# Kernel tuning notes

Measured on AMD Instinct MI355X. Metric: run time of the kernel, lower is better.

The kernel has to match this reference:

```python
import jax, jax.numpy as jnp
import numpy as np

N = 8192


def setup_inputs() -> dict:
    key = jax.random.key(0)
    ks = jax.random.split(key, 12)
    H_emb = jax.random.normal(ks[0], (645, 1140), jnp.float32) * 0.05
    H_emb = H_emb.at[0].set(0.0)  # padding_idx=0
    inp = {
        "ld_gcn": jax.random.normal(ks[1], (N, 512), jnp.float32),
        "ld_encoder": jax.random.normal(ks[2], (N, 512), jnp.float32),
        "x": jax.random.randint(ks[3], (N,), 0, 240),
        "y": jax.random.randint(ks[4], (N,), 0, 404),
        "H_emb": H_emb,
        "conv_w": jax.random.normal(ks[5], (32, 1, 2, 25), jnp.float32) * (1.0 / np.sqrt(2 * 25)),
        "conv_b": jnp.zeros((32,), jnp.float32),
        "W1": jax.random.normal(ks[6], (1000, 3968), jnp.float32) * (1.0 / np.sqrt(3968)),
        "b1": jnp.zeros((1000,), jnp.float32),
        "W2": jax.random.normal(ks[7], (100, 1000), jnp.float32) * (1.0 / np.sqrt(1000)),
        "b2": jnp.zeros((100,), jnp.float32),
        "Wg": jax.random.normal(ks[8], (100, 512), jnp.float32) * (1.0 / np.sqrt(512)),
        "bg": jnp.zeros((100,), jnp.float32),
        "We": jax.random.normal(ks[9], (100, 512), jnp.float32) * (1.0 / np.sqrt(512)),
        "be": jnp.zeros((100,), jnp.float32),
    }
    return inp


def reference(ld_gcn, ld_encoder, x, y, H_emb, conv_w, conv_b, W1, b1, W2, b2, Wg, bg, We, be):
    n = x.shape[0]
    lrelu = lambda t: jax.nn.leaky_relu(t, 0.01)
    # embedding lookups + concat -> (n,1,2,1140)
    h = jnp.concatenate([H_emb[x], H_emb[y + 240]], axis=1).reshape(n, 1, 2, 1140)
    # CNN: conv (2,25) stride (1,9) valid -> (n,32,1,124)
    c = jax.lax.conv_general_dilated(h, conv_w, window_strides=(1, 9), padding="VALID",
                                     dimension_numbers=("NCHW", "OIHW", "NCHW"))
    c = lrelu(c + conv_b[None, :, None, None]).reshape(n, -1)  # (n,3968)
    # fc_H (dropout = identity at eval)
    hfc = lrelu(c @ W1.T + b1)
    hfc = lrelu(hfc @ W2.T + b2)  # (n,100)
    # gating projections
    g = jnp.tanh(ld_gcn @ Wg.T + bg)       # (n,100)
    e = jnp.tanh(ld_encoder @ We.T + be)   # (n,100)
    # diagonal of (n,100)@(100,n) == row-wise dot product
    a_gcn = jnp.einsum("nd,nd->n", g, hfc)
    a_enc = jnp.einsum("nd,nd->n", e, hfc)
    att = jax.nn.softmax(jnp.stack([a_gcn, a_enc], axis=1), axis=1)  # (n,2)
    return ld_gcn * att[:, :1], ld_encoder * att[:, 1:]
```

## Files before the change

### kernel.cpp

```cpp
#include <hip/hip_runtime.h>
#include <hip/hip_bf16.h>

typedef unsigned short u16;
typedef short bf16x8 __attribute__((ext_vector_type(8)));
typedef float f32x4 __attribute__((ext_vector_type(4)));

#define NROWS 8192
#define EMBD  1140
#define FDIM  3968
#define N1R   1000
#define N1P   1024
#define N2R   100
#define N2P   128
#define DG    512

__device__ inline u16 f2b(float f) {
  __hip_bfloat16 h = __float2bfloat16(f);
  return *reinterpret_cast<u16*>(&h);
}

__device__ inline float b2f(u16 u) {
  unsigned v = (unsigned)u << 16;
  union { unsigned u; float f; } c;
  c.u = v;
  return c.f;
}

__device__ inline float tanh_fast(float x) {
  float ax = fabsf(x);
  float t = __expf(-2.f * ax);
  float r = (1.f - t) / (1.f + t);
  return x < 0.f ? -r : r;
}

__device__ inline void gld16(const void* g, void* l) {
  __builtin_amdgcn_global_load_lds(
      (const __attribute__((address_space(1))) unsigned int*)g,
      (__attribute__((address_space(3))) unsigned int*)l, 16, 0, 0);
}

__global__ __launch_bounds__(256) void prep_kernel(
    const float* __restrict__ W1, const float* __restrict__ W2,
    const float* __restrict__ Wg, const float* __restrict__ We,
    const float* __restrict__ H_emb, const float* __restrict__ conv_w,
    const float* __restrict__ conv_b,
    u16* __restrict__ W1bf, u16* __restrict__ W2bf,
    u16* __restrict__ Wgbf, u16* __restrict__ Webf,
    u16* __restrict__ Abuf, u16* __restrict__ Bbuf) {
  const int b = blockIdx.x;
  const int t = threadIdx.x;
  if (b < 2112) {
    const float* src;
    u16* dst;
    int row, c8, realRow, realCol;
    if (b < 1984) {
      int id = b * 256 + t;
      row = id / 496; c8 = (id - row * 496) * 8;
      src = W1 + (size_t)row * FDIM + c8;
      dst = W1bf + (size_t)row * FDIM + c8;
      realRow = N1R; realCol = FDIM;
    } else if (b < 2048) {
      int id = (b - 1984) * 256 + t;
      row = id >> 7; c8 = (id & 127) * 8;
      src = W2 + (size_t)row * N1R + c8;
      dst = W2bf + (size_t)row * N1P + c8;
      realRow = N2R; realCol = N1R;
    } else if (b < 2080) {
      int id = (b - 2048) * 256 + t;
      row = id >> 6; c8 = (id & 63) * 8;
      src = Wg + (size_t)row * DG + c8;
      dst = Wgbf + (size_t)row * DG + c8;
      realRow = N2R; realCol = DG;
    } else {
      int id = (b - 2080) * 256 + t;
      row = id >> 6; c8 = (id & 63) * 8;
      src = We + (size_t)row * DG + c8;
      dst = Webf + (size_t)row * DG + c8;
      realRow = N2R; realCol = DG;
    }
    bf16x8 o = (bf16x8){0, 0, 0, 0, 0, 0, 0, 0};
    if (row < realRow && c8 < realCol) {
#pragma unroll
      for (int j = 0; j < 8; ++j) o[j] = (short)f2b(src[j]);
    }
    *(bf16x8*)dst = o;
    return;
  }
  __shared__ float se[EMBD];
  __shared__ float sw[32 * 25];
  __shared__ float sb[32];
  const int eb = b - 2112;
  bool isA = eb < 240;
  const float* emb = H_emb + (size_t)eb * EMBD;
  u16* outp = isA ? (Abuf + (size_t)eb * FDIM) : (Bbuf + (size_t)(eb - 240) * FDIM);
  for (int i = t; i < EMBD; i += 256) se[i] = emb[i];
  int kh = isA ? 0 : 1;
  for (int i = t; i < 800; i += 256) {
    int o = i / 25, kw = i - o * 25;
    sw[i] = conv_w[o * 50 + kh * 25 + kw];
  }
  if (t < 32) sb[t] = isA ? conv_b[t] : 0.f;
  __syncthreads();
  for (int f = t; f < FDIM; f += 256) {
    int o = f / 124, wpos = f - o * 124;
    const float* e = se + wpos * 9;
    const float* wp = sw + o * 25;
    float acc = sb[o];
#pragma unroll
    for (int kw = 0; kw < 25; ++kw) acc += wp[kw] * e[kw];
    outp[f] = f2b(acc);
  }
}

__global__ __launch_bounds__(256) void conv_combine_kernel(
    const u16* __restrict__ Abuf, const u16* __restrict__ Bbuf,
    const int* __restrict__ xi, const int* __restrict__ yi, u16* __restrict__ cbf) {
  int r = blockIdx.x;
  const bf16x8* pa = (const bf16x8*)(Abuf + (size_t)xi[r] * FDIM);
  const bf16x8* pb = (const bf16x8*)(Bbuf + (size_t)yi[r] * FDIM);
  bf16x8* out = (bf16x8*)(cbf + (size_t)r * FDIM);
  for (int i = threadIdx.x; i < FDIM / 8; i += 256) {
    bf16x8 a = pa[i], b = pb[i];
    bf16x8 o;
#pragma unroll
    for (int j = 0; j < 8; ++j) {
      float v = b2f((u16)a[j]) + b2f((u16)b[j]);
      v = v > 0.f ? v : 0.01f * v;
      o[j] = (short)f2b(v);
    }
    out[i] = o;
  }
}

__global__ __launch_bounds__(256) void fc1_kernel(
    const u16* __restrict__ A, const u16* __restrict__ B,
    const float* __restrict__ bias, int realN,
    u16* __restrict__ C, int K, int ldc, int nTilesX) {
  const int nwg = gridDim.x;
  const int cpx = nwg >> 3;
  const int bid = blockIdx.x;
  const int wg = (bid & 7) * cpx + (bid >> 3);
  const int tm = (wg / nTilesX) * 128;
  const int tn = (wg % nTilesX) * 128;

  __shared__ u16 As[2][8192];
  __shared__ u16 Bs[2][8192];
  const int t = threadIdx.x;
  const int lane = t & 63;
  const int w = t >> 6;
  const int wr = (w >> 1) * 64, wc = (w & 1) * 64;
  const int fr = lane & 15;
  const int kg = lane >> 4;

  const int srow = lane >> 3;
  const int su = ((lane & 7) ^ srow) * 8;
  const u16* gA[4];
  const u16* gB[4];
  int ldsOff[4];
#pragma unroll
  for (int i = 0; i < 4; ++i) {
    const int c = w + i * 4;
    gA[i] = A + (size_t)(tm + c * 8 + srow) * K + su;
    gB[i] = B + (size_t)(tn + c * 8 + srow) * K + su;
    ldsOff[i] = c * 512;
  }

  f32x4 acc[4][4];
#pragma unroll
  for (int m = 0; m < 4; ++m)
#pragma unroll
    for (int n = 0; n < 4; ++n) acc[m][n] = (f32x4){0.f, 0.f, 0.f, 0.f};

  const int nk = K >> 6;
#pragma unroll
  for (int i = 0; i < 4; ++i) {
    gld16(gA[i], &As[0][ldsOff[i]]);
    gld16(gB[i], &Bs[0][ldsOff[i]]);
  }
  __syncthreads();

  for (int kt = 0; kt < nk; ++kt) {
    const int cb = kt & 1;
    if (kt + 1 < nk) {
      const int ko = (kt + 1) << 6;
#pragma unroll
      for (int i = 0; i < 4; ++i) {
        gld16(gA[i] + ko, &As[cb ^ 1][ldsOff[i]]);
        gld16(gB[i] + ko, &Bs[cb ^ 1][ldsOff[i]]);
      }
    }
    __builtin_amdgcn_sched_barrier(0);
#pragma unroll
    for (int ks = 0; ks < 2; ++ks) {
      const int un = ((ks * 4 + kg) ^ (fr & 7)) << 4;
      bf16x8 af[4], bff[4];
#pragma unroll
      for (int m = 0; m < 4; ++m)
        af[m] = *(const bf16x8*)((const char*)As[cb] + (wr + m * 16 + fr) * 128 + un);
#pragma unroll
      for (int n = 0; n < 4; ++n)
        bff[n] = *(const bf16x8*)((const char*)Bs[cb] + (wc + n * 16 + fr) * 128 + un);
#pragma unroll
      for (int m = 0; m < 4; ++m)
#pragma unroll
        for (int n = 0; n < 4; ++n)
          acc[m][n] = __builtin_amdgcn_mfma_f32_16x16x32_bf16(af[m], bff[n], acc[m][n], 0, 0, 0);
    }
    __syncthreads();
  }

#pragma unroll
  for (int n = 0; n < 4; ++n) {
    int col = tn + wc + n * 16 + fr;
    float bv = (col < realN) ? bias[col] : 0.f;
#pragma unroll
    for (int m = 0; m < 4; ++m) {
#pragma unroll
      for (int j = 0; j < 4; ++j) {
        int row = tm + wr + m * 16 + kg * 4 + j;
        float v = acc[m][n][j] + bv;
        v = v > 0.f ? v : 0.01f * v;
        C[(size_t)row * ldc + col] = f2b(v);
      }
    }
  }
}

__global__ __launch_bounds__(256) void tail_kernel(
    const u16* __restrict__ hfc1, const u16* __restrict__ W2bf, const float* __restrict__ b2,
    const float* __restrict__ ldg, const float* __restrict__ lde,
    const u16* __restrict__ Wgbf, const float* __restrict__ bg,
    const u16* __restrict__ Webf, const float* __restrict__ be,
    float* __restrict__ out0, float* __restrict__ out1) {
  __shared__ float H16[N2P][16];
  __shared__ float dpart[2][4][16];
  __shared__ float wt[2][16];

  const int tm = blockIdx.x * 16;
  const int t = threadIdx.x;
  const int lane = t & 63;
  const int w = t >> 6;
  const int fr = lane & 15;
  const int kg = lane >> 4;
  const int n0 = w * 2;

  {
    f32x4 a0 = (f32x4){0.f, 0.f, 0.f, 0.f}, a1 = a0;
    const u16* Ap = hfc1 + (size_t)(tm + fr) * N1P + kg * 8;
    const u16* B0 = W2bf + (size_t)(n0 * 16 + fr) * N1P + kg * 8;
    const u16* B1 = B0 + (size_t)16 * N1P;
#pragma unroll 8
    for (int kt = 0; kt < N1P / 32; ++kt) {
      bf16x8 af = *(const bf16x8*)(Ap + kt * 32);
      bf16x8 f0 = *(const bf16x8*)(B0 + kt * 32);
      bf16x8 f1 = *(const bf16x8*)(B1 + kt * 32);
      a0 = __builtin_amdgcn_mfma_f32_16x16x32_bf16(af, f0, a0, 0, 0, 0);
      a1 = __builtin_amdgcn_mfma_f32_16x16x32_bf16(af, f1, a1, 0, 0, 0);
    }
#pragma unroll
    for (int n = 0; n < 2; ++n) {
      int col = (n0 + n) * 16 + fr;
      float bv = (col < N2R) ? b2[col] : 0.f;
      f32x4 v = n == 0 ? a0 : a1;
      f32x4 o;
#pragma unroll
      for (int j = 0; j < 4; ++j) {
        float x = v[j] + bv;
        o[j] = x > 0.f ? x : 0.01f * x;
      }
      *(f32x4*)&H16[col][kg * 4] = o;
    }
  }
  __syncthreads();

#pragma unroll 1
  for (int sec = 0; sec < 2; ++sec) {
    const float* ld = sec == 0 ? ldg : lde;
    const u16* Wb = sec == 0 ? Wgbf : Webf;
    const float* bb = sec == 0 ? bg : be;

    f32x4 a0 = (f32x4){0.f, 0.f, 0.f, 0.f}, a1 = a0;
    const float* Ap = ld + (size_t)(tm + fr) * DG + kg * 8;
    const u16* B0 = Wb + (size_t)(n0 * 16 + fr) * DG + kg * 8;
    const u16* B1 = B0 + (size_t)16 * DG;
#pragma unroll 4
    for (int kt = 0; kt < DG / 32; ++kt) {
      float4 v0 = *(const float4*)(Ap + kt * 32);
      float4 v1 = *(const float4*)(Ap + kt * 32 + 4);
      bf16x8 af;
      af[0] = (short)f2b(v0.x); af[1] = (short)f2b(v0.y);
      af[2] = (short)f2b(v0.z); af[3] = (short)f2b(v0.w);
      af[4] = (short)f2b(v1.x); af[5] = (short)f2b(v1.y);
      af[6] = (short)f2b(v1.z); af[7] = (short)f2b(v1.w);
      bf16x8 f0 = *(const bf16x8*)(B0 + kt * 32);
      bf16x8 f1 = *(const bf16x8*)(B1 + kt * 32);
      a0 = __builtin_amdgcn_mfma_f32_16x16x32_bf16(af, f0, a0, 0, 0, 0);
      a1 = __builtin_amdgcn_mfma_f32_16x16x32_bf16(af, f1, a1, 0, 0, 0);
    }
    float dv[4] = {0.f, 0.f, 0.f, 0.f};
#pragma unroll
    for (int n = 0; n < 2; ++n) {
      int col = (n0 + n) * 16 + fr;
      float bv = (col < N2R) ? bb[col] : 0.f;
      f32x4 v = n == 0 ? a0 : a1;
      f32x4 h = *(const f32x4*)&H16[col][kg * 4];
#pragma unroll
      for (int j = 0; j < 4; ++j)
        dv[j] += tanh_fast(v[j] + bv) * h[j];
    }
#pragma unroll
    for (int j = 0; j < 4; ++j) {
      float v = dv[j];
      v += __shfl_xor(v, 1);
      v += __shfl_xor(v, 2);
      v += __shfl_xor(v, 4);
      v += __shfl_xor(v, 8);
      dv[j] = v;
    }
    if (fr == 0) {
#pragma unroll
      for (int j = 0; j < 4; ++j) dpart[sec][w][kg * 4 + j] = dv[j];
    }
  }
  __syncthreads();

  if (t < 16) {
    float ag = dpart[0][0][t] + dpart[0][1][t] + dpart[0][2][t] + dpart[0][3][t];
    float ae = dpart[1][0][t] + dpart[1][1][t] + dpart[1][2][t] + dpart[1][3][t];
    float mm = fmaxf(ag, ae);
    float eg = __expf(ag - mm), eo = __expf(ae - mm);
    float inv = 1.f / (eg + eo);
    wt[0][t] = eg * inv;
    wt[1][t] = eo * inv;
  }
  __syncthreads();

  for (int i = t; i < 16 * (DG / 4); i += 256) {
    int r = i >> 7, c = i & 127;
    float w0 = wt[0][r], w1 = wt[1][r];
    size_t off = (size_t)(tm + r) * DG + c * 4;
    float4 a = *(const float4*)(ldg + off);
    a.x *= w0; a.y *= w0; a.z *= w0; a.w *= w0;
    *(float4*)(out0 + off) = a;
    float4 b = *(const float4*)(lde + off);
    b.x *= w1; b.y *= w1; b.z *= w1; b.w *= w1;
    *(float4*)(out1 + off) = b;
  }
}

extern "C" void kernel_launch(void* const* d_in, const int* in_sizes, int n_in,
                              void* d_out, int out_size, void* d_ws, size_t ws_size,
                              hipStream_t stream) {
  const float* ld_gcn = (const float*)d_in[0];
  const float* ld_enc = (const float*)d_in[1];
  const int*   xi     = (const int*)d_in[2];
  const int*   yi     = (const int*)d_in[3];
  const float* H_emb  = (const float*)d_in[4];
  const float* conv_w = (const float*)d_in[5];
  const float* conv_b = (const float*)d_in[6];
  const float* W1     = (const float*)d_in[7];
  const float* b1     = (const float*)d_in[8];
  const float* W2     = (const float*)d_in[9];
  const float* b2     = (const float*)d_in[10];
  const float* Wg     = (const float*)d_in[11];
  const float* bg     = (const float*)d_in[12];
  const float* We     = (const float*)d_in[13];
  const float* be     = (const float*)d_in[14];

  char* ws = (char*)d_ws;
  size_t off = 0;
  auto alloc = [&](size_t bytes) -> void* {
    void* p = ws + off;
    off = (off + bytes + 255) & ~(size_t)255;
    return p;
  };
  u16* Abuf = (u16*)alloc(240ull * FDIM * 2);
  u16* Bbuf = (u16*)alloc(404ull * FDIM * 2);
  u16* cbf  = (u16*)alloc((size_t)NROWS * FDIM * 2);
  u16* W1bf = (u16*)alloc((size_t)N1P * FDIM * 2);
  u16* W2bf = (u16*)alloc((size_t)N2P * N1P * 2);
  u16* Wgbf = (u16*)alloc((size_t)N2P * DG * 2);
  u16* Webf = (u16*)alloc((size_t)N2P * DG * 2);
  u16* hfc1 = (u16*)alloc((size_t)NROWS * N1P * 2);
  if (ws_size < off) return;

  prep_kernel<<<2756, 256, 0, stream>>>(W1, W2, Wg, We, H_emb, conv_w, conv_b,
                                        W1bf, W2bf, Wgbf, Webf, Abuf, Bbuf);
  conv_combine_kernel<<<NROWS, 256, 0, stream>>>(Abuf, Bbuf, xi, yi, cbf);

  fc1_kernel<<<dim3((NROWS / 128) * (N1P / 128)), 256, 0, stream>>>(
      cbf, W1bf, b1, N1R, hfc1, FDIM, N1P, N1P / 128);

  float* out0 = (float*)d_out;
  float* out1 = out0 + (size_t)NROWS * DG;
  tail_kernel<<<NROWS / 16, 256, 0, stream>>>(
      hfc1, W2bf, b2, ld_gcn, ld_enc, Wgbf, bg, Webf, be, out0, out1);
}
```

Baseline: 182.5 us.

## Fuse embedding-conv gather and combine into fc1 GEMM A-tile loading

Removes the separate conv_combine kernel and its 8192x3968 bf16 intermediate by having the fc1 GEMM gather the per-index conv partials from Abuf/Bbuf, add them, apply leaky-relu, and write the A tile into LDS. Global loads of the next A tile go to registers, are combined after the MFMA loop, and are stored to the alternate LDS buffer. This saves a round trip of about 65MB through HBM and one kernel launch. In exchange each A element is now gathered and recombined once per N-tile (8 times), register pressure rises, and the direct global-to-LDS path for A becomes register staging.

Result: slower. 210.4 us (+15.3%).

```diff
diff --git a/kernel.cpp b/kernel.cpp
--- a/kernel.cpp
+++ b/kernel.cpp
@@ -31,6 +31,17 @@
   float t = __expf(-2.f * ax);
   float r = (1.f - t) / (1.f + t);
   return x < 0.f ? -r : r;
+}
+
+__device__ inline bf16x8 combine8(bf16x8 a, bf16x8 b) {
+  bf16x8 o;
+#pragma unroll
+  for (int j = 0; j < 8; ++j) {
+    float v = b2f((u16)a[j]) + b2f((u16)b[j]);
+    v = v > 0.f ? v : 0.01f * v;
+    o[j] = (short)f2b(v);
+  }
+  return o;
 }
 
 __device__ inline void gld16(const void* g, void* l) {
@@ -112,28 +123,10 @@
   }
 }
 
-__global__ __launch_bounds__(256) void conv_combine_kernel(
+__global__ __launch_bounds__(256) void fc1_kernel(
     const u16* __restrict__ Abuf, const u16* __restrict__ Bbuf,
-    const int* __restrict__ xi, const int* __restrict__ yi, u16* __restrict__ cbf) {
-  int r = blockIdx.x;
-  const bf16x8* pa = (const bf16x8*)(Abuf + (size_t)xi[r] * FDIM);
-  const bf16x8* pb = (const bf16x8*)(Bbuf + (size_t)yi[r] * FDIM);
-  bf16x8* out = (bf16x8*)(cbf + (size_t)r * FDIM);
-  for (int i = threadIdx.x; i < FDIM / 8; i += 256) {
-    bf16x8 a = pa[i], b = pb[i];
-    bf16x8 o;
-#pragma unroll
-    for (int j = 0; j < 8; ++j) {
-      float v = b2f((u16)a[j]) + b2f((u16)b[j]);
-      v = v > 0.f ? v : 0.01f * v;
-      o[j] = (short)f2b(v);
-    }
-    out[i] = o;
-  }
-}
-
-__global__ __launch_bounds__(256) void fc1_kernel(
-    const u16* __restrict__ A, const u16* __restrict__ B,
+    const int* __restrict__ xi, const int* __restrict__ yi,
+    const u16* __restrict__ B,
     const float* __restrict__ bias, int realN,
     u16* __restrict__ C, int K, int ldc, int nTilesX) {
   const int nwg = gridDim.x;
@@ -154,13 +147,16 @@
 
   const int srow = lane >> 3;
   const int su = ((lane & 7) ^ srow) * 8;
-  const u16* gA[4];
+  const u16* pA[4];
+  const u16* pB[4];
   const u16* gB[4];
   int ldsOff[4];
 #pragma unroll
   for (int i = 0; i < 4; ++i) {
     const int c = w + i * 4;
-    gA[i] = A + (size_t)(tm + c * 8 + srow) * K + su;
+    const int row = tm + c * 8 + srow;
+    pA[i] = Abuf + (size_t)xi[row] * FDIM + su;
+    pB[i] = Bbuf + (size_t)yi[row] * FDIM + su;
     gB[i] = B + (size_t)(tn + c * 8 + srow) * K + su;
     ldsOff[i] = c * 512;
   }
@@ -172,11 +168,16 @@
     for (int n = 0; n < 4; ++n) acc[m][n] = (f32x4){0.f, 0.f, 0.f, 0.f};
 
   const int nk = K >> 6;
+  bf16x8 ra[4], rb[4];
 #pragma unroll
   for (int i = 0; i < 4; ++i) {
-    gld16(gA[i], &As[0][ldsOff[i]]);
+    ra[i] = *(const bf16x8*)(pA[i]);
+    rb[i] = *(const bf16x8*)(pB[i]);
     gld16(gB[i], &Bs[0][ldsOff[i]]);
   }
+#pragma unroll
+  for (int i = 0; i < 4; ++i)
+    *(bf16x8*)(&As[0][ldsOff[i] + lane * 8]) = combine8(ra[i], rb[i]);
   __syncthreads();
 
   for (int kt = 0; kt < nk; ++kt) {
@@ -185,7 +186,8 @@
       const int ko = (kt + 1) << 6;
 #pragma unroll
       for (int i = 0; i < 4; ++i) {
-        gld16(gA[i] + ko, &As[cb ^ 1][ldsOff[i]]);
+        ra[i] = *(const bf16x8*)(pA[i] + ko);
+        rb[i] = *(const bf16x8*)(pB[i] + ko);
         gld16(gB[i] + ko, &Bs[cb ^ 1][ldsOff[i]]);
       }
     }
@@ -205,6 +207,11 @@
 #pragma unroll
         for (int n = 0; n < 4; ++n)
           acc[m][n] = __builtin_amdgcn_mfma_f32_16x16x32_bf16(af[m], bff[n], acc[m][n], 0, 0, 0);
+    }
+    if (kt + 1 < nk) {
+#pragma unroll
+      for (int i = 0; i < 4; ++i)
+        *(bf16x8*)(&As[cb ^ 1][ldsOff[i] + lane * 8]) = combine8(ra[i], rb[i]);
     }
     __syncthreads();
   }
@@ -376,7 +383,6 @@
   };
   u16* Abuf = (u16*)alloc(240ull * FDIM * 2);
   u16* Bbuf = (u16*)alloc(404ull * FDIM * 2);
-  u16* cbf  = (u16*)alloc((size_t)NROWS * FDIM * 2);
   u16* W1bf = (u16*)alloc((size_t)N1P * FDIM * 2);
   u16* W2bf = (u16*)alloc((size_t)N2P * N1P * 2);
   u16* Wgbf = (u16*)alloc((size_t)N2P * DG * 2);
@@ -386,10 +392,9 @@
 
   prep_kernel<<<2756, 256, 0, stream>>>(W1, W2, Wg, We, H_emb, conv_w, conv_b,
                                         W1bf, W2bf, Wgbf, Webf, Abuf, Bbuf);
-  conv_combine_kernel<<<NROWS, 256, 0, stream>>>(Abuf, Bbuf, xi, yi, cbf);
 
   fc1_kernel<<<dim3((NROWS / 128) * (N1P / 128)), 256, 0, stream>>>(
-      cbf, W1bf, b1, N1R, hfc1, FDIM, N1P, N1P / 128);
+      Abuf, Bbuf, xi, yi, W1bf, b1, N1R, hfc1, FDIM, N1P, N1P / 128);
 
   float* out0 = (float*)d_out;
   float* out1 = out0 + (size_t)NROWS * DG;
```
